# Optimization experiments

Hardware: AMD Instinct MI355X
Metric: run time of the kernel (lower is better)

## Reference

```python
import jax, jax.numpy as jnp
import numpy as np

B, T, H, V, C = 8192, 40, 128, 4450, 102

def setup_inputs() -> dict:
    key = jax.random.key(0)
    ks = jax.random.split(key, 9)
    s = 1.0 / np.sqrt(H)
    return {
        "input_ids": jax.random.randint(ks[0], (B, T), 0, V, dtype=jnp.int64),
        "emb_c": jax.random.normal(ks[1], (V, H), jnp.float32),
        "emb_a": jax.random.normal(ks[2], (V, H), jnp.float32),
        "W_ih": jax.random.uniform(ks[3], (3 * H, H), jnp.float32, -s, s),
        "W_hh": jax.random.uniform(ks[4], (3 * H, H), jnp.float32, -s, s),
        "b_ih": jax.random.uniform(ks[5], (3 * H,), jnp.float32, -s, s),
        "b_hh": jax.random.uniform(ks[6], (3 * H,), jnp.float32, -s, s),
        "W_cls": jax.random.uniform(ks[7], (C, H), jnp.float32, -s, s),
        "b_cls": jax.random.uniform(ks[8], (C,), jnp.float32, -s, s),
    }

def _gru_scan(x_seq, W_ih, W_hh, b_ih, b_hh):
    # x_seq: [T, B, H]; PyTorch GRU gate order: r, z, n
    h0 = jnp.zeros((x_seq.shape[1], H), x_seq.dtype)
    def step(h, x):
        gi = x @ W_ih.T + b_ih          # [B, 3H]
        gh = h @ W_hh.T + b_hh          # [B, 3H]
        i_r, i_z, i_n = jnp.split(gi, 3, axis=-1)
        h_r, h_z, h_n = jnp.split(gh, 3, axis=-1)
        r = jax.nn.sigmoid(i_r + h_r)
        z = jax.nn.sigmoid(i_z + h_z)
        n = jnp.tanh(i_n + r * h_n)
        h_new = (1.0 - z) * n + z * h
        return h_new, h_new
    _, hs = jax.lax.scan(step, h0, x_seq)
    return hs                            # [T, B, H]

def reference(input_ids, emb_c, emb_a, W_ih, W_hh, b_ih, b_hh, W_cls, b_cls):
    x_a = emb_a[input_ids].transpose(1, 0, 2)   # [T, B, H]
    x_c = emb_c[input_ids].transpose(1, 0, 2)
    ha = _gru_scan(x_a, W_ih, W_hh, b_ih, b_hh).transpose(1, 0, 2)  # [B, T, H]
    hc = _gru_scan(x_c, W_ih, W_hh, b_ih, b_hh).transpose(1, 0, 2)
    matrix = jnp.einsum('bth,bsh->bts', ha, ha)  # [B, T, T]
    A = jax.nn.softmax(matrix, axis=1)           # Softmax(dim=1) over 3D
    attn = A.transpose(0, 2, 1)                  # [B, T, T]
    # bmm(hc^T [B,H,T], attn).transpose -> out[b,s,h] = sum_t hc[b,t,h]*attn[b,t,s]
    out = jnp.einsum('bth,bts->bsh', hc, attn)   # [B, T, H]
    logits = out.reshape(-1, H) @ W_cls.T + b_cls  # [B*T, C]
    return jax.nn.softmax(logits, axis=1)
```

## Files before the change

### kernel.cpp

```cpp
#include <hip/hip_runtime.h>
#include <hip/hip_bf16.h>

#define BB 8192
#define TT 40
#define HH 128
#define CC 102
#define VV 4450

#define L2E  1.4426950408889634f
#define L2E2 2.8853900817779268f

typedef __attribute__((ext_vector_type(8))) short short8;
typedef __attribute__((ext_vector_type(4))) float f4;

__device__ __forceinline__ float rcpf_(float x) { return __builtin_amdgcn_rcpf(x); }
__device__ __forceinline__ float exp2f_(float x) { return __builtin_amdgcn_exp2f(x); }

__device__ __forceinline__ void barrier_lds() {
    asm volatile("s_waitcnt lgkmcnt(0)\n\ts_barrier" ::: "memory");
}

__device__ __forceinline__ unsigned short f2bf(float x) {
    union { float f; unsigned u; } v; v.f = x;
    unsigned r = v.u + 0x7FFFu + ((v.u >> 16) & 1u);
    return (unsigned short)(r >> 16);
}
__device__ __forceinline__ float bf2f(unsigned short h) {
    union { float f; unsigned u; } v; v.u = ((unsigned)h) << 16; return v.f;
}
__device__ __forceinline__ short8 u4s8(uint4 v) { return *(short8*)&v; }

__device__ __forceinline__ unsigned cvtpk_bf16(float lo, float hi) {
    unsigned r;
    asm("v_cvt_pk_bf16_f32 %0, %1, %2" : "=v"(r) : "v"(lo), "v"(hi));
    return r;
}
__device__ __forceinline__ void split2(float a, float b, unsigned& H, unsigned& L) {
    H = cvtpk_bf16(a, b);
    float ra = __uint_as_float(H << 16);
    float rb = __uint_as_float(H & 0xFFFF0000u);
    L = cvtpk_bf16(a - ra, b - rb);
}

struct __attribute__((aligned(4))) G3 { float r, z, n; };

#define MFMA16(acc, a, b) acc = __builtin_amdgcn_mfma_f32_16x16x32_bf16(a, b, acc, 0, 0, 0)

__global__ __launch_bounds__(256) void prep_bf16split(const float* __restrict__ W,
                                                      unsigned short* __restrict__ hi,
                                                      unsigned short* __restrict__ lo, int n) {
    int i = blockIdx.x * 256 + threadIdx.x;
    if (i < n) {
        float x = W[i];
        unsigned short h = f2bf(x);
        hi[i] = h;
        lo[i] = f2bf(x - bf2f(h));
    }
}

__global__ __launch_bounds__(256) void prep_whh(const float* __restrict__ W,
                                                unsigned short* __restrict__ hi,
                                                unsigned short* __restrict__ lo) {
    int i = blockIdx.x * 256 + threadIdx.x;
    if (i < 384 * HH) {
        float s = (i < 256 * HH) ? L2E : L2E2;
        float x = W[i] * s;
        unsigned short h = f2bf(x);
        hi[i] = h;
        lo[i] = f2bf(x - bf2f(h));
    }
}

__global__ __launch_bounds__(256) void prep_wcls(const float* __restrict__ W,
                                                 unsigned short* __restrict__ hi,
                                                 unsigned short* __restrict__ lo) {
    int i = blockIdx.x * 256 + threadIdx.x;
    if (i < 112 * HH) {
        int r = i >> 7;
        float x = (r < CC) ? W[i] : 0.f;
        unsigned short h = f2bf(x);
        hi[i] = h;
        lo[i] = f2bf(x - bf2f(h));
    }
}

__global__ __launch_bounds__(256) void prep_G_mfma(
    const float* __restrict__ emb_a, const float* __restrict__ emb_c,
    const unsigned short* __restrict__ WihH, const unsigned short* __restrict__ WihL,
    const float* __restrict__ b_ih, const float* __restrict__ b_hh,
    float* __restrict__ G)
{
    __shared__ uint4 se[2][32][16];

    const int tid = threadIdx.x;
    const int src = blockIdx.y;
    const float* emb = src ? emb_c : emb_a;
    const int v0 = blockIdx.x * 32;

    const int lane = tid & 63;
    const int w = tid >> 6;
    const int mcol = lane & 15;
    const int quad = lane >> 4;

#pragma unroll
    for (int i = 0; i < 4; ++i) {
        int task = tid + 256 * i;
        int row = task >> 5, q = task & 31;
        int v = v0 + row;
        float4 x = make_float4(0.f, 0.f, 0.f, 0.f);
        if (v < VV) x = ((const float4*)(emb + (size_t)v * HH))[q];
        uint2 Hw, Lw;
        split2(x.x, x.y, Hw.x, Lw.x);
        split2(x.z, x.w, Hw.y, Lw.y);
        int phys = (q >> 1) ^ (row & 15);
        ((uint2*)&se[0][row][phys])[q & 1] = Hw;
        ((uint2*)&se[1][row][phys])[q & 1] = Lw;
    }

    float bias[6];
#pragma unroll
    for (int n6 = 0; n6 < 6; ++n6) {
        int c = w * 96 + n6 * 16 + mcol;
        bias[n6] = b_ih[c] + (c < 256 ? b_hh[c] : 0.f);
    }

    f4 acc[2][6];
#pragma unroll
    for (int mt = 0; mt < 2; ++mt)
#pragma unroll
        for (int n6 = 0; n6 < 6; ++n6) acc[mt][n6] = (f4){0.f, 0.f, 0.f, 0.f};

    __syncthreads();

#pragma unroll
    for (int kk = 0; kk < 4; ++kk) {
        uint4 bH[6], bL[6];
#pragma unroll
        for (int n6 = 0; n6 < 6; ++n6) {
            int rowc = w * 96 + n6 * 16 + mcol;
            bH[n6] = *((const uint4*)WihH + rowc * 16 + kk * 4 + quad);
            bL[n6] = *((const uint4*)WihL + rowc * 16 + kk * 4 + quad);
        }
#pragma unroll
        for (int mt = 0; mt < 2; ++mt) {
            int m = mt * 16 + mcol;
            int phys = (kk * 4 + quad) ^ mcol;
            short8 ah = u4s8(se[0][m][phys]);
            short8 al = u4s8(se[1][m][phys]);
#pragma unroll
            for (int n6 = 0; n6 < 6; ++n6) {
                MFMA16(acc[mt][n6], ah, u4s8(bH[n6]));
                MFMA16(acc[mt][n6], ah, u4s8(bL[n6]));
                MFMA16(acc[mt][n6], al, u4s8(bH[n6]));
            }
        }
    }

    float* gout = G + (size_t)src * VV * 384;
#pragma unroll
    for (int mt = 0; mt < 2; ++mt)
#pragma unroll
        for (int r = 0; r < 4; ++r) {
            int m = mt * 16 + quad * 4 + r;
            int v = v0 + m;
            if (v < VV) {
#pragma unroll
                for (int n6 = 0; n6 < 6; ++n6) {
                    int c = w * 96 + n6 * 16 + mcol;
                    int g = c >> 7, jj = c & 127;
                    float scl = (g < 2) ? L2E : L2E2;
                    gout[(size_t)v * 384 + jj * 3 + g] = (acc[mt][n6][r] + bias[n6]) * scl;
                }
            }
        }
}

__global__ __launch_bounds__(512, 2) void gru_mfma(
    const int* __restrict__ ids, const float* __restrict__ G,
    const __hip_bfloat16* __restrict__ Whi, const __hip_bfloat16* __restrict__ Wlo,
    const float* __restrict__ b_hh, float* __restrict__ ha, float* __restrict__ hc)
{
    __shared__ uint4 sh[2][2][32][16];
    __shared__ int sids[32 * TT];

    const int tid = threadIdx.x;
    const int src = blockIdx.x & 1;
    const int b0 = (blockIdx.x >> 1) * 32;
    const float* Gs = G + (size_t)src * VV * 384;
    float* hout = src ? hc : ha;

    const int lane = tid & 63;
    const int w = tid >> 6;
    const int nc0 = w * 16;
    const int mcol = lane & 15;
    const int quad = lane >> 4;

    for (int idx = tid; idx < 32 * TT; idx += 512)
        sids[idx] = ids[b0 * TT + idx];

    {
        uint4 z; z.x = z.y = z.z = z.w = 0u;
        uint4* p = &sh[0][0][0][0];
        for (int idx = tid; idx < 2 * 32 * 16; idx += 512) p[idx] = z;
    }

    short8 bh[3][4], bl[3][4];
#pragma unroll
    for (int g = 0; g < 3; ++g)
#pragma unroll
        for (int kk = 0; kk < 4; ++kk) {
            int row = g * 128 + nc0 + mcol;
            uint4 vh = *((const uint4*)Whi + row * 16 + kk * 4 + quad);
            uint4 vl = *((const uint4*)Wlo + row * 16 + kk * 4 + quad);
            bh[g][kk] = u4s8(vh);
            bl[g][kk] = u4s8(vl);
        }

    const int j = nc0 + mcol;
    const float bhn = L2E2 * b_hh[256 + j];
    const float* gbase = Gs + 3 * j;

    f4 hreg[2];
    hreg[0] = (f4){0.f, 0.f, 0.f, 0.f};
    hreg[1] = (f4){0.f, 0.f, 0.f, 0.f};

    __syncthreads();

    G3 gc[2][4];
#pragma unroll
    for (int mt = 0; mt < 2; ++mt)
#pragma unroll
        for (int reg = 0; reg < 4; ++reg) {
            int m = mt * 16 + quad * 4 + reg;
            int id = sids[m * TT + 0];
            gc[mt][reg] = *(const G3*)(gbase + (size_t)id * 384);
        }

    const int s_slot = j >> 3;
    const int jb = j & 7;

    int buf = 0;
#pragma unroll 1
    for (int t = 0; t < TT; ++t) {
        f4 acc[3][2];
#pragma unroll
        for (int g = 0; g < 3; ++g)
#pragma unroll
            for (int mt = 0; mt < 2; ++mt) acc[g][mt] = (f4){0.f, 0.f, 0.f, 0.f};

#pragma unroll
        for (int mt = 0; mt < 2; ++mt)
#pragma unroll
            for (int kk = 0; kk < 4; ++kk) {
                int m = mt * 16 + mcol;
                int phys = (kk * 4 + quad) ^ mcol;
                uint4 avh = sh[buf][0][m][phys];
                uint4 avl = sh[buf][1][m][phys];
                short8 ah = u4s8(avh), al = u4s8(avl);
#pragma unroll
                for (int g = 0; g < 3; ++g) {
                    MFMA16(acc[g][mt], ah, bh[g][kk]);
                    MFMA16(acc[g][mt], ah, bl[g][kk]);
                    MFMA16(acc[g][mt], al, bh[g][kk]);
                }
            }

        const int nbuf = buf ^ 1;
#pragma unroll
        for (int mt = 0; mt < 2; ++mt) {
            float hv4[4];
#pragma unroll
            for (int reg = 0; reg < 4; ++reg) {
                G3 g = gc[mt][reg];
                float rr = rcpf_(1.f + exp2f_(-(acc[0][mt][reg] + g.r)));
                float zz = rcpf_(1.f + exp2f_(-(acc[1][mt][reg] + g.z)));
                float y  = g.n + rr * (acc[2][mt][reg] + bhn);
                float nn = 1.f - 2.f * rcpf_(exp2f_(y) + 1.f);
                float hv = fmaf(zz, hreg[mt][reg] - nn, nn);
                hreg[mt][reg] = hv;
                hv4[reg] = hv;

                int m = mt * 16 + quad * 4 + reg;
                hout[((size_t)(b0 + m) * TT + t) * HH + j] = hv;
            }
#pragma unroll
            for (int pr = 0; pr < 2; ++pr) {
                unsigned Hp, Lp;
                split2(hv4[pr * 2], hv4[pr * 2 + 1], Hp, Lp);
#pragma unroll
                for (int k = 0; k < 2; ++k) {
                    int m = mt * 16 + quad * 4 + pr * 2 + k;
                    int phys = s_slot ^ (m & 15);
                    unsigned short hb = (unsigned short)(k ? (Hp >> 16) : Hp);
                    unsigned short lb = (unsigned short)(k ? (Lp >> 16) : Lp);
                    ((unsigned short*)&sh[nbuf][0][m][phys])[jb] = hb;
                    ((unsigned short*)&sh[nbuf][1][m][phys])[jb] = lb;
                }
            }
        }

        if (t < TT - 1) {
#pragma unroll
            for (int mt = 0; mt < 2; ++mt)
#pragma unroll
                for (int reg = 0; reg < 4; ++reg) {
                    int m = mt * 16 + quad * 4 + reg;
                    int id = sids[m * TT + t + 1];
                    gc[mt][reg] = *(const G3*)(gbase + (size_t)id * 384);
                }
        }
        barrier_lds();
        buf ^= 1;
    }
}

#define AT_SHA     0
#define AT_SHA_LO  12288
#define AT_SHCT    24576
#define AT_SHCT_LO 40960
#define AT_SM      57344
#define AT_SW      66752
#define AT_SW_LO   72896
#define AT_PARTM   79040
#define AT_PARTD   79808
#define AT_SMX     80576
#define AT_SDI     80768
#define AT_TOTAL   80960

__global__ __launch_bounds__(256, 2) void attn_cls_mfma(
    const float* __restrict__ ha, const float* __restrict__ hc,
    const unsigned short* __restrict__ WcH, const unsigned short* __restrict__ WcL,
    const float* __restrict__ b_cls, float* __restrict__ out)
{
    __shared__ __attribute__((aligned(16))) char smem[AT_TOTAL];
    const int tid = threadIdx.x;
    const int lane = tid & 63;
    const int w = tid >> 6;
    const int quad = lane >> 4;
    const int col = lane & 15;
    const size_t b = blockIdx.x;

    float* sm    = (float*)(smem + AT_SM);
    float* slog  = (float*)(smem + AT_SM);
    float* partM = (float*)(smem + AT_PARTM);
    float* partD = (float*)(smem + AT_PARTD);
    float* sMX   = (float*)(smem + AT_SMX);
    float* sDI   = (float*)(smem + AT_SDI);

    const int ntc0 = (w < 3) ? w : 3;
    const int ntc1 = (w < 3) ? w + 4 : 3;
    uint4 bw[2][4][2];
    float bcv[2];
    {
        int nts[2] = {ntc0, ntc1};
#pragma unroll
        for (int which = 0; which < 2; ++which) {
            int row = nts[which] * 16 + col;
#pragma unroll
            for (int kk = 0; kk < 4; ++kk) {
                bw[which][kk][0] = *((const uint4*)WcH + row * 16 + kk * 4 + quad);
                bw[which][kk][1] = *((const uint4*)WcL + row * 16 + kk * 4 + quad);
            }
            bcv[which] = (row < CC) ? b_cls[row] : 0.f;
        }
    }

    {
        const float4* hab = (const float4*)(ha + b * TT * HH);
#pragma unroll
        for (int i = 0; i < 5; ++i) {
            int f4i = tid + 256 * i;
            int row = f4i >> 5, q = f4i & 31;
            float4 v = hab[f4i];
            uint2 Hw, Lw;
            split2(v.x, v.y, Hw.x, Lw.x);
            split2(v.z, v.w, Hw.y, Lw.y);
            int phys = (q >> 1) ^ (row & 15);
            int off = row * 256 + phys * 16 + (q & 1) * 8;
            *(uint2*)(smem + AT_SHA + off) = Hw;
            *(uint2*)(smem + AT_SHA_LO + off) = Lw;
        }
        if (tid < 128) {
            int row = 40 + (tid >> 4), c = tid & 15;
            uint4 z; z.x = z.y = z.z = z.w = 0u;
            *(uint4*)(smem + AT_SHA + row * 256 + c * 16) = z;
            *(uint4*)(smem + AT_SHA_LO + row * 256 + c * 16) = z;
        }
        const float* hcb = hc + b * TT * HH;
        for (int task = tid; task < 640; task += 256) {
            int h = task & 127, c = task >> 7;
            float x[8];
#pragma unroll
            for (int jj = 0; jj < 8; ++jj) x[jj] = hcb[(c * 8 + jj) * HH + h];
            uint4 Hq, Lq;
            split2(x[0], x[1], Hq.x, Lq.x);
            split2(x[2], x[3], Hq.y, Lq.y);
            split2(x[4], x[5], Hq.z, Lq.z);
            split2(x[6], x[7], Hq.w, Lq.w);
            int phys = c ^ (h & 7);
            *(uint4*)(smem + AT_SHCT + h * 128 + phys * 16) = Hq;
            *(uint4*)(smem + AT_SHCT_LO + h * 128 + phys * 16) = Lq;
        }
        for (int task = tid; task < 384; task += 256) {
            int h = task & 127, c = 5 + (task >> 7);
            int phys = c ^ (h & 7);
            uint4 z; z.x = z.y = z.z = z.w = 0u;
            *(uint4*)(smem + AT_SHCT + h * 128 + phys * 16) = z;
            *(uint4*)(smem + AT_SHCT_LO + h * 128 + phys * 16) = z;
        }
    }
    __syncthreads();

    if (w < 3) {
        const int mt = w;
        uint4 aH[4], aL[4];
#pragma unroll
        for (int kk = 0; kk < 4; ++kk) {
            int phys = (kk * 4 + quad) ^ col;
            int off = (mt * 16 + col) * 256 + phys * 16;
            aH[kk] = *(uint4*)(smem + AT_SHA + off);
            aL[kk] = *(uint4*)(smem + AT_SHA_LO + off);
        }
        f4 acc[3];
#pragma unroll
        for (int nt = 0; nt < 3; ++nt) acc[nt] = (f4){0.f, 0.f, 0.f, 0.f};
#pragma unroll
        for (int kk = 0; kk < 4; ++kk) {
            short8 ah = u4s8(aH[kk]), al = u4s8(aL[kk]);
#pragma unroll
            for (int nt = 0; nt < 3; ++nt) {
                int phys = (kk * 4 + quad) ^ col;
                int off = (nt * 16 + col) * 256 + phys * 16;
                short8 bH = u4s8(*(uint4*)(smem + AT_SHA + off));
                short8 bL = u4s8(*(uint4*)(smem + AT_SHA_LO + off));
                MFMA16(acc[nt], ah, bH);
                MFMA16(acc[nt], ah, bL);
                MFMA16(acc[nt], al, bH);
            }
        }
#pragma unroll
        for (int nt = 0; nt < 3; ++nt)
#pragma unroll
            for (int r = 0; r < 4; ++r)
                sm[(mt * 16 + quad * 4 + r) * 49 + nt * 16 + col] = acc[nt][r];
    }
    __syncthreads();

    if (tid < 160) {
        int t = tid >> 2, p = tid & 3;
        const float* row = sm + t * 49 + p * 10;
        float M = row[0];
#pragma unroll
        for (int i = 1; i < 10; ++i) M = fmaxf(M, row[i]);
        float D = 0.f;
#pragma unroll
        for (int i = 0; i < 10; ++i) D += __expf(row[i] - M);
        partM[t * 4 + p] = M;
        partD[t * 4 + p] = D;
    }
    __syncthreads();
    if (tid < 40) {
        float M = partM[tid * 4];
        M = fmaxf(M, partM[tid * 4 + 1]); M = fmaxf(M, partM[tid * 4 + 2]); M = fmaxf(M, partM[tid * 4 + 3]);
        float D = 0.f;
#pragma unroll
        for (int p = 0; p < 4; ++p) D += partD[tid * 4 + p] * __expf(partM[tid * 4 + p] - M);
        sMX[tid] = M;
        sDI[tid] = rcpf_(D);
    }
    __syncthreads();

    for (int task = tid; task < 384; task += 256) {
        int s = task >> 3, c = task & 7;
        uint4 Hq, Lq;
        if (c >= 5) {
            Hq.x = Hq.y = Hq.z = Hq.w = 0u; Lq = Hq;
        } else {
            const float* srow = sm + s * 49 + c * 8;
            float wv[8];
#pragma unroll
            for (int jj = 0; jj < 8; ++jj) {
                int t = c * 8 + jj;
                wv[jj] = __expf(srow[jj] - sMX[t]) * sDI[t];
            }
            split2(wv[0], wv[1], Hq.x, Lq.x);
            split2(wv[2], wv[3], Hq.y, Lq.y);
            split2(wv[4], wv[5], Hq.z, Lq.z);
            split2(wv[6], wv[7], Hq.w, Lq.w);
        }
        int phys = c ^ (s & 7);
        *(uint4*)(smem + AT_SW + s * 128 + phys * 16) = Hq;
        *(uint4*)(smem + AT_SW_LO + s * 128 + phys * 16) = Lq;
    }
    __syncthreads();

    {
        uint4 aH[3][2], aL[3][2];
#pragma unroll
        for (int mt = 0; mt < 3; ++mt)
#pragma unroll
            for (int kk = 0; kk < 2; ++kk) {
                int s = mt * 16 + col;
                int phys = (kk * 4 + quad) ^ (s & 7);
                aH[mt][kk] = *(uint4*)(smem + AT_SW + s * 128 + phys * 16);
                aL[mt][kk] = *(uint4*)(smem + AT_SW_LO + s * 128 + phys * 16);
            }
        f4 acc[3][2];
#pragma unroll
        for (int mt = 0; mt < 3; ++mt) { acc[mt][0] = (f4){0,0,0,0}; acc[mt][1] = (f4){0,0,0,0}; }
#pragma unroll
        for (int which = 0; which < 2; ++which) {
            int nt = w + which * 4;
            int hrow = nt * 16 + col;
#pragma unroll
            for (int kk = 0; kk < 2; ++kk) {
                int phys = (kk * 4 + quad) ^ (hrow & 7);
                short8 bH = u4s8(*(uint4*)(smem + AT_SHCT + hrow * 128 + phys * 16));
                short8 bL = u4s8(*(uint4*)(smem + AT_SHCT_LO + hrow * 128 + phys * 16));
#pragma unroll
                for (int mt = 0; mt < 3; ++mt) {
                    short8 ah = u4s8(aH[mt][kk]), al = u4s8(aL[mt][kk]);
                    MFMA16(acc[mt][which], ah, bH);
                    MFMA16(acc[mt][which], ah, bL);
                    MFMA16(acc[mt][which], al, bH);
                }
            }
        }
        __syncthreads();
#pragma unroll
        for (int which = 0; which < 2; ++which) {
            int h = (w + which * 4) * 16 + col;
            int chunk = h >> 3, hb7 = (h & 7) * 2;
#pragma unroll
            for (int mt = 0; mt < 3; ++mt)
#pragma unroll
                for (int pr = 0; pr < 2; ++pr) {
                    unsigned Hp, Lp;
                    split2(acc[mt][which][pr * 2], acc[mt][which][pr * 2 + 1], Hp, Lp);
#pragma unroll
                    for (int k = 0; k < 2; ++k) {
                        int s = mt * 16 + quad * 4 + pr * 2 + k;
                        int phys = chunk ^ (s & 15);
                        *(unsigned short*)(smem + AT_SHA + s * 256 + phys * 16 + hb7) =
                            (unsigned short)(k ? (Hp >> 16) : Hp);
                        *(unsigned short*)(smem + AT_SHA_LO + s * 256 + phys * 16 + hb7) =
                            (unsigned short)(k ? (Lp >> 16) : Lp);
                    }
                }
        }
    }
    __syncthreads();

    {
        f4 acc[3][2];
#pragma unroll
        for (int mt = 0; mt < 3; ++mt) { acc[mt][0] = (f4){0,0,0,0}; acc[mt][1] = (f4){0,0,0,0}; }
#pragma unroll
        for (int kk = 0; kk < 4; ++kk)
#pragma unroll
            for (int mt = 0; mt < 3; ++mt) {
                int s = mt * 16 + col;
                int phys = (kk * 4 + quad) ^ (s & 15);
                short8 ah = u4s8(*(uint4*)(smem + AT_SHA + s * 256 + phys * 16));
                short8 al = u4s8(*(uint4*)(smem + AT_SHA_LO + s * 256 + phys * 16));
#pragma unroll
                for (int which = 0; which < 2; ++which) {
                    MFMA16(acc[mt][which], ah, u4s8(bw[which][kk][0]));
                    MFMA16(acc[mt][which], ah, u4s8(bw[which][kk][1]));
                    MFMA16(acc[mt][which], al, u4s8(bw[which][kk][0]));
                }
            }
        __syncthreads();
        int nts[2] = {ntc0, ntc1};
#pragma unroll
        for (int which = 0; which < 2; ++which) {
            int c = nts[which] * 16 + col;
#pragma unroll
            for (int mt = 0; mt < 3; ++mt)
#pragma unroll
                for (int r = 0; r < 4; ++r)
                    slog[(mt * 16 + quad * 4 + r) * 113 + c] = acc[mt][which][r] + bcv[which];
        }
    }
    __syncthreads();

    if (tid < 160) {
        int s = tid >> 2, p = tid & 3;
        int c0 = p * 26;
        int c1 = (c0 + 26 < CC) ? c0 + 26 : CC;
        const float* row = slog + s * 113;
        float M = row[c0];
        for (int c = c0 + 1; c < c1; ++c) M = fmaxf(M, row[c]);
        float D = 0.f;
        for (int c = c0; c < c1; ++c) D += __expf(row[c] - M);
        partM[s * 4 + p] = M;
        partD[s * 4 + p] = D;
    }
    __syncthreads();
    if (tid < 40) {
        float M = partM[tid * 4];
        M = fmaxf(M, partM[tid * 4 + 1]); M = fmaxf(M, partM[tid * 4 + 2]); M = fmaxf(M, partM[tid * 4 + 3]);
        float D = 0.f;
#pragma unroll
        for (int p = 0; p < 4; ++p) D += partD[tid * 4 + p] * __expf(partM[tid * 4 + p] - M);
        sMX[tid] = M;
        sDI[tid] = rcpf_(D);
    }
    __syncthreads();

    {
        int c = tid & 127, s0 = tid >> 7;
        if (c < CC) {
            float* ob = out + b * TT * CC;
            for (int s = s0; s < TT; s += 2)
                ob[s * CC + c] = __expf(slog[s * 113 + c] - sMX[s]) * sDI[s];
        }
    }
}

extern "C" void kernel_launch(void* const* d_in, const int* in_sizes, int n_in,
                              void* d_out, int out_size, void* d_ws, size_t ws_size,
                              hipStream_t stream) {
    const int*   ids   = (const int*)d_in[0];
    const float* emb_c = (const float*)d_in[1];
    const float* emb_a = (const float*)d_in[2];
    const float* W_ih  = (const float*)d_in[3];
    const float* W_hh  = (const float*)d_in[4];
    const float* b_ih  = (const float*)d_in[5];
    const float* b_hh  = (const float*)d_in[6];
    const float* W_cls = (const float*)d_in[7];
    const float* b_cls = (const float*)d_in[8];
    float* out = (float*)d_out;

    float* ha = (float*)d_ws;
    float* hc = ha + (size_t)BB * TT * HH;
    float* G  = hc + (size_t)BB * TT * HH;
    __hip_bfloat16* Whi = (__hip_bfloat16*)(G + (size_t)2 * VV * 384);
    __hip_bfloat16* Wlo = Whi + 384 * HH;
    unsigned short* WcH = (unsigned short*)(Wlo + 384 * HH);
    unsigned short* WcL = WcH + 112 * HH;
    unsigned short* WihH = WcL + 112 * HH;
    unsigned short* WihL = WihH + 384 * HH;

    prep_whh<<<(384 * HH + 255) / 256, 256, 0, stream>>>(W_hh, (unsigned short*)Whi, (unsigned short*)Wlo);
    prep_bf16split<<<(384 * HH + 255) / 256, 256, 0, stream>>>(W_ih, WihH, WihL, 384 * HH);
    prep_wcls<<<(112 * HH + 255) / 256, 256, 0, stream>>>(W_cls, WcH, WcL);
    prep_G_mfma<<<dim3((VV + 31) / 32, 2), 256, 0, stream>>>(emb_a, emb_c, WihH, WihL, b_ih, b_hh, G);
    gru_mfma<<<dim3(BB / 32 * 2), 512, 0, stream>>>(ids, G, Whi, Wlo, b_hh, ha, hc);
    attn_cls_mfma<<<BB, 256, 0, stream>>>(ha, hc, WcH, WcL, b_cls, out);
}
```

Baseline: 588.7 us.

## Alias shared-memory regions in attention kernel to fit three blocks per CU

```diff
diff --git a/kernel.cpp b/kernel.cpp
--- a/kernel.cpp
+++ b/kernel.cpp
@@ -314,20 +314,24 @@
     }
 }
 
-#define AT_SHA     0
-#define AT_SHA_LO  12288
-#define AT_SHCT    24576
-#define AT_SHCT_LO 40960
-#define AT_SM      57344
-#define AT_SW      66752
-#define AT_SW_LO   72896
-#define AT_PARTM   79040
-#define AT_PARTD   79808
-#define AT_SMX     80576
-#define AT_SDI     80768
-#define AT_TOTAL   80960
-
-__global__ __launch_bounds__(256, 2) void attn_cls_mfma(
+#define AT_HA      0
+#define AT_HA_LO   12288
+#define AT_HCT     0
+#define AT_HCT_LO  16384
+#define AT_PV      0
+#define AT_PV_LO   12288
+#define AT_SM      32768
+#define AT_SW      40608
+#define AT_SW_LO   45728
+#define AT_ZROW    50848
+#define AT_SLOG    32768
+#define AT_PARTM   50976
+#define AT_PARTD   51616
+#define AT_SMX     52256
+#define AT_SDI     52416
+#define AT_TOTAL   52576
+
+__global__ __launch_bounds__(256, 3) void attn_cls_mfma(
     const float* __restrict__ ha, const float* __restrict__ hc,
     const unsigned short* __restrict__ WcH, const unsigned short* __restrict__ WcL,
     const float* __restrict__ b_cls, float* __restrict__ out)
@@ -341,7 +345,7 @@
     const size_t b = blockIdx.x;
 
     float* sm    = (float*)(smem + AT_SM);
-    float* slog  = (float*)(smem + AT_SM);
+    float* slog  = (float*)(smem + AT_SLOG);
     float* partM = (float*)(smem + AT_PARTM);
     float* partD = (float*)(smem + AT_PARTD);
     float* sMX   = (float*)(smem + AT_SMX);
@@ -377,15 +381,57 @@
             split2(v.z, v.w, Hw.y, Lw.y);
             int phys = (q >> 1) ^ (row & 15);
             int off = row * 256 + phys * 16 + (q & 1) * 8;
-            *(uint2*)(smem + AT_SHA + off) = Hw;
-            *(uint2*)(smem + AT_SHA_LO + off) = Lw;
-        }
+            *(uint2*)(smem + AT_HA + off) = Hw;
+            *(uint2*)(smem + AT_HA_LO + off) = Lw;
+        }
+        uint4 z; z.x = z.y = z.z = z.w = 0u;
         if (tid < 128) {
             int row = 40 + (tid >> 4), c = tid & 15;
-            uint4 z; z.x = z.y = z.z = z.w = 0u;
-            *(uint4*)(smem + AT_SHA + row * 256 + c * 16) = z;
-            *(uint4*)(smem + AT_SHA_LO + row * 256 + c * 16) = z;
-        }
+            *(uint4*)(smem + AT_HA + row * 256 + c * 16) = z;
+            *(uint4*)(smem + AT_HA_LO + row * 256 + c * 16) = z;
+        }
+        if (tid < 8) ((uint4*)(smem + AT_ZROW))[tid] = z;
+    }
+    __syncthreads();
+
+    if (w < 3) {
+        const int mt = w;
+        uint4 aH[4], aL[4];
+#pragma unroll
+        for (int kk = 0; kk < 4; ++kk) {
+            int phys = (kk * 4 + quad) ^ col;
+            int off = (mt * 16 + col) * 256 + phys * 16;
+            aH[kk] = *(uint4*)(smem + AT_HA + off);
+            aL[kk] = *(uint4*)(smem + AT_HA_LO + off);
+        }
+        f4 acc[3];
+#pragma unroll
+        for (int nt = 0; nt < 3; ++nt) acc[nt] = (f4){0.f, 0.f, 0.f, 0.f};
+#pragma unroll
+        for (int kk = 0; kk < 4; ++kk) {
+            short8 ah = u4s8(aH[kk]), al = u4s8(aL[kk]);
+#pragma unroll
+            for (int nt = 0; nt < 3; ++nt) {
+                int phys = (kk * 4 + quad) ^ col;
+                int off = (nt * 16 + col) * 256 + phys * 16;
+                short8 bH = u4s8(*(uint4*)(smem + AT_HA + off));
+                short8 bL = u4s8(*(uint4*)(smem + AT_HA_LO + off));
+                MFMA16(acc[nt], ah, bH);
+                MFMA16(acc[nt], ah, bL);
+                MFMA16(acc[nt], al, bH);
+            }
+        }
+#pragma unroll
+        for (int nt = 0; nt < 3; ++nt)
+#pragma unroll
+            for (int r = 0; r < 4; ++r) {
+                int row = mt * 16 + quad * 4 + r;
+                if (row < 40) sm[row * 49 + nt * 16 + col] = acc[nt][r];
+            }
+    }
+    __syncthreads();
+
+    {
         const float* hcb = hc + b * TT * HH;
         for (int task = tid; task < 640; task += 256) {
             int h = task & 127, c = task >> 7;
@@ -398,54 +444,17 @@
             split2(x[4], x[5], Hq.z, Lq.z);
             split2(x[6], x[7], Hq.w, Lq.w);
             int phys = c ^ (h & 7);
-            *(uint4*)(smem + AT_SHCT + h * 128 + phys * 16) = Hq;
-            *(uint4*)(smem + AT_SHCT_LO + h * 128 + phys * 16) = Lq;
+            *(uint4*)(smem + AT_HCT + h * 128 + phys * 16) = Hq;
+            *(uint4*)(smem + AT_HCT_LO + h * 128 + phys * 16) = Lq;
         }
         for (int task = tid; task < 384; task += 256) {
             int h = task & 127, c = 5 + (task >> 7);
             int phys = c ^ (h & 7);
             uint4 z; z.x = z.y = z.z = z.w = 0u;
-            *(uint4*)(smem + AT_SHCT + h * 128 + phys * 16) = z;
-            *(uint4*)(smem + AT_SHCT_LO + h * 128 + phys * 16) = z;
-        }
-    }
-    __syncthreads();
-
-    if (w < 3) {
-        const int mt = w;
-        uint4 aH[4], aL[4];
-#pragma unroll
-        for (int kk = 0; kk < 4; ++kk) {
-            int phys = (kk * 4 + quad) ^ col;
-            int off = (mt * 16 + col) * 256 + phys * 16;
-            aH[kk] = *(uint4*)(smem + AT_SHA + off);
-            aL[kk] = *(uint4*)(smem + AT_SHA_LO + off);
-        }
-        f4 acc[3];
-#pragma unroll
-        for (int nt = 0; nt < 3; ++nt) acc[nt] = (f4){0.f, 0.f, 0.f, 0.f};
-#pragma unroll
-        for (int kk = 0; kk < 4; ++kk) {
-            short8 ah = u4s8(aH[kk]), al = u4s8(aL[kk]);
-#pragma unroll
-            for (int nt = 0; nt < 3; ++nt) {
-                int phys = (kk * 4 + quad) ^ col;
-                int off = (nt * 16 + col) * 256 + phys * 16;
-                short8 bH = u4s8(*(uint4*)(smem + AT_SHA + off));
-                short8 bL = u4s8(*(uint4*)(smem + AT_SHA_LO + off));
-                MFMA16(acc[nt], ah, bH);
-                MFMA16(acc[nt], ah, bL);
-                MFMA16(acc[nt], al, bH);
-            }
-        }
-#pragma unroll
-        for (int nt = 0; nt < 3; ++nt)
-#pragma unroll
-            for (int r = 0; r < 4; ++r)
-                sm[(mt * 16 + quad * 4 + r) * 49 + nt * 16 + col] = acc[nt][r];
-    }
-    __syncthreads();
-
+            *(uint4*)(smem + AT_HCT + h * 128 + phys * 16) = z;
+            *(uint4*)(smem + AT_HCT_LO + h * 128 + phys * 16) = z;
+        }
+    }
     if (tid < 160) {
         int t = tid >> 2, p = tid & 3;
         const float* row = sm + t * 49 + p * 10;
@@ -470,7 +479,7 @@
     }
     __syncthreads();
 
-    for (int task = tid; task < 384; task += 256) {
+    for (int task = tid; task < 320; task += 256) {
         int s = task >> 3, c = task & 7;
         uint4 Hq, Lq;
         if (c >= 5) {
@@ -502,8 +511,13 @@
             for (int kk = 0; kk < 2; ++kk) {
                 int s = mt * 16 + col;
                 int phys = (kk * 4 + quad) ^ (s & 7);
-                aH[mt][kk] = *(uint4*)(smem + AT_SW + s * 128 + phys * 16);
-                aL[mt][kk] = *(uint4*)(smem + AT_SW_LO + s * 128 + phys * 16);
+                if (s < 40) {
+                    aH[mt][kk] = *(uint4*)(smem + AT_SW + s * 128 + phys * 16);
+                    aL[mt][kk] = *(uint4*)(smem + AT_SW_LO + s * 128 + phys * 16);
+                } else {
+                    aH[mt][kk] = *(uint4*)(smem + AT_ZROW + phys * 16);
+                    aL[mt][kk] = aH[mt][kk];
+                }
             }
         f4 acc[3][2];
 #pragma unroll
@@ -515,8 +529,8 @@
 #pragma unroll
             for (int kk = 0; kk < 2; ++kk) {
                 int phys = (kk * 4 + quad) ^ (hrow & 7);
-                short8 bH = u4s8(*(uint4*)(smem + AT_SHCT + hrow * 128 + phys * 16));
-                short8 bL = u4s8(*(uint4*)(smem + AT_SHCT_LO + hrow * 128 + phys * 16));
+                short8 bH = u4s8(*(uint4*)(smem + AT_HCT + hrow * 128 + phys * 16));
+                short8 bL = u4s8(*(uint4*)(smem + AT_HCT_LO + hrow * 128 + phys * 16));
 #pragma unroll
                 for (int mt = 0; mt < 3; ++mt) {
                     short8 ah = u4s8(aH[mt][kk]), al = u4s8(aL[mt][kk]);
@@ -541,9 +555,9 @@
                     for (int k = 0; k < 2; ++k) {
                         int s = mt * 16 + quad * 4 + pr * 2 + k;
                         int phys = chunk ^ (s & 15);
-                        *(unsigned short*)(smem + AT_SHA + s * 256 + phys * 16 + hb7) =
+                        *(unsigned short*)(smem + AT_PV + s * 256 + phys * 16 + hb7) =
                             (unsigned short)(k ? (Hp >> 16) : Hp);
-                        *(unsigned short*)(smem + AT_SHA_LO + s * 256 + phys * 16 + hb7) =
+                        *(unsigned short*)(smem + AT_PV_LO + s * 256 + phys * 16 + hb7) =
                             (unsigned short)(k ? (Lp >> 16) : Lp);
                     }
                 }
@@ -561,8 +575,8 @@
             for (int mt = 0; mt < 3; ++mt) {
                 int s = mt * 16 + col;
                 int phys = (kk * 4 + quad) ^ (s & 15);
-                short8 ah = u4s8(*(uint4*)(smem + AT_SHA + s * 256 + phys * 16));
-                short8 al = u4s8(*(uint4*)(smem + AT_SHA_LO + s * 256 + phys * 16));
+                short8 ah = u4s8(*(uint4*)(smem + AT_PV + s * 256 + phys * 16));
+                short8 al = u4s8(*(uint4*)(smem + AT_PV_LO + s * 256 + phys * 16));
 #pragma unroll
                 for (int which = 0; which < 2; ++which) {
                     MFMA16(acc[mt][which], ah, u4s8(bw[which][kk][0]));
@@ -578,8 +592,10 @@
 #pragma unroll
             for (int mt = 0; mt < 3; ++mt)
 #pragma unroll
-                for (int r = 0; r < 4; ++r)
-                    slog[(mt * 16 + quad * 4 + r) * 113 + c] = acc[mt][which][r] + bcv[which];
+                for (int r = 0; r < 4; ++r) {
+                    int row = mt * 16 + quad * 4 + r;
+                    if (row < 40) slog[row * 113 + c] = acc[mt][which][r] + bcv[which];
+                }
         }
     }
     __syncthreads();
```

After: 549.3 us. -6.7%, faster.
